# Performance work log

Measured on AMD Instinct MI355X. Metric: run time of the kernel, lower is better.

Reference implementation:

```python
import jax, jax.numpy as jnp
import numpy as np
import math

B, T, F, H = 8, 1024, 1024, 16
D = F // H

def setup_inputs() -> dict:
    key = jax.random.key(0)
    ks = jax.random.split(key, 6)
    s = 1.0 / math.sqrt(F)
    return {
        "qkv": jax.random.normal(ks[0], (B, T, F), dtype=jnp.float32),
        "key_padding_mask": jax.random.randint(ks[1], (B, T), 0, 2).astype(bool),
        "in_proj_w": jax.random.normal(ks[2], (3 * F, F), dtype=jnp.float32) * s,
        "in_proj_b": jax.random.normal(ks[3], (3 * F,), dtype=jnp.float32) * 0.02,
        "out_proj_w": jax.random.normal(ks[4], (F, F), dtype=jnp.float32) * s,
        "out_proj_b": jax.random.normal(ks[5], (F,), dtype=jnp.float32) * 0.02,
    }

def reference(qkv, key_padding_mask, in_proj_w, in_proj_b, out_proj_w, out_proj_b):
    b, t, f = qkv.shape
    h, d = H, f // H
    norm = jnp.asarray(math.sqrt(d), dtype=qkv.dtype)
    # fused QKV projection (torch Linear: x @ W.T + b)
    x = qkv @ in_proj_w.T + in_proj_b                     # [B, T, 3F]
    q, k, v = jnp.split(x, 3, axis=-1)
    q = q.reshape(b, t, h, d).transpose(0, 2, 1, 3)       # [B, H, T, D]
    k = k.reshape(b, t, h, d).transpose(0, 2, 1, 3)
    v = v.reshape(b, t, h, d).transpose(0, 2, 1, 3)
    dot = jnp.einsum("bhqd,bhkd->bhqk", q, k) / norm      # [B, H, T, T]
    dot = jnp.where(key_padding_mask[:, None, None, :], -jnp.inf, dot)
    alpha = jax.nn.softmax(dot, axis=-1)                  # [B, H, T, T]
    att = jnp.einsum("bhqk,bhkd->bhqd", alpha, v)         # [B, H, T, D]
    att = att.transpose(0, 2, 1, 3).reshape(b, t, f)      # [B, T, F]
    out = att @ out_proj_w.T + out_proj_b
    return (out, alpha)
```

## Files before the change

kernel.cpp:

```cpp
#include <hip/hip_runtime.h>
#include <math.h>

#define B_ 8
#define T_ 1024
#define F_ 1024
#define H_ 16
#define D_ 64

typedef __bf16 bf16x8 __attribute__((ext_vector_type(8)));
typedef float f32x4 __attribute__((ext_vector_type(4)));
typedef unsigned short u16x8 __attribute__((ext_vector_type(8)));

__device__ __forceinline__ unsigned short f2bf(float f) {
    union { float f; unsigned u; } v; v.f = f;
    unsigned r = v.u + 0x7fffu + ((v.u >> 16) & 1u);
    return (unsigned short)(r >> 16);
}

__device__ __forceinline__ void gld16(const void* g, void* l) {
    __builtin_amdgcn_global_load_lds(
        (const __attribute__((address_space(1))) void*)g,
        (__attribute__((address_space(3))) void*)l, 16, 0, 0);
}

__device__ __forceinline__ int swz4(int row15) {
    return (row15 ^ (row15 >> 2)) & 3;
}

__global__ __launch_bounds__(256) void cvt_f32_bf16(
    const float* __restrict__ in, unsigned short* __restrict__ out, int n8)
{
    int i = blockIdx.x * 256 + threadIdx.x;
    if (i >= n8) return;
    const float4* p = (const float4*)in + (size_t)i * 2;
    float4 x = p[0], y = p[1];
    u16x8 o;
    o[0] = f2bf(x.x); o[1] = f2bf(x.y); o[2] = f2bf(x.z); o[3] = f2bf(x.w);
    o[4] = f2bf(y.x); o[5] = f2bf(y.y); o[6] = f2bf(y.z); o[7] = f2bf(y.w);
    ((u16x8*)out)[i] = o;
}

__global__ __launch_bounds__(256) void qkv_gemm(
    const unsigned short* __restrict__ A,
    const unsigned short* __restrict__ Bw,
    const float* __restrict__ bias,
    unsigned short* __restrict__ qb,
    unsigned short* __restrict__ kb,
    unsigned short* __restrict__ vb)
{
    __shared__ __align__(16) unsigned short As[128 * 32];
    __shared__ __align__(16) unsigned short Bs[128 * 32];
    const int K = 1024;
    int tid = threadIdx.x;
    int lane = tid & 63, wave = tid >> 6;
    int wr = wave >> 1, wc = wave & 1;
    int m0 = blockIdx.y * 128, n0 = blockIdx.x * 128;
    int col = lane & 15, quad = lane >> 4;
    int sw = swz4(col);
    int rl = lane >> 2;
    int lc = (lane & 3) ^ swz4(rl);

    f32x4 acc[4][4] = {};
    for (int kc = 0; kc < K; kc += 32) {
        __syncthreads();
        #pragma unroll
        for (int l = 0; l < 2; l++) {
            int ia = wave * 2 + l;
            gld16(A  + (size_t)(m0 + ia * 16 + rl) * K + kc + lc * 8, &As[ia * 512]);
            gld16(Bw + (size_t)(n0 + ia * 16 + rl) * K + kc + lc * 8, &Bs[ia * 512]);
        }
        __syncthreads();
        bf16x8 af[4], bg[4];
        #pragma unroll
        for (int mt = 0; mt < 4; mt++)
            af[mt] = *(const bf16x8*)&As[(wr * 64 + mt * 16 + col) * 32 + ((quad ^ sw)) * 8];
        #pragma unroll
        for (int nt = 0; nt < 4; nt++)
            bg[nt] = *(const bf16x8*)&Bs[(wc * 64 + nt * 16 + col) * 32 + ((quad ^ sw)) * 8];
        #pragma unroll
        for (int mt = 0; mt < 4; mt++)
            #pragma unroll
            for (int nt = 0; nt < 4; nt++)
                acc[mt][nt] = __builtin_amdgcn_mfma_f32_16x16x32_bf16(
                    af[mt], bg[nt], acc[mt][nt], 0, 0, 0);
    }
    int which = n0 >> 10;
    #pragma unroll
    for (int nt = 0; nt < 4; nt++) {
        int n = n0 + wc * 64 + nt * 16 + col;
        int hn = (n & 1023) >> 6, d = n & 63;
        float bn = bias[n];
        #pragma unroll
        for (int mt = 0; mt < 4; mt++) {
            #pragma unroll
            for (int r = 0; r < 4; r++) {
                int m = m0 + wr * 64 + mt * 16 + quad * 4 + r;
                int bb = m >> 10, t = m & 1023;
                unsigned short bf = f2bf(acc[mt][nt][r] + bn);
                if (which == 0)
                    qb[(size_t)((bb * H_ + hn) * T_ + t) * D_ + d] = bf;
                else if (which == 1)
                    kb[(size_t)((bb * H_ + hn) * T_ + t) * D_ + d] = bf;
                else
                    vb[(size_t)((bb * H_ + hn) * D_ + d) * T_ + t] = bf;
            }
        }
    }
}

__global__ __launch_bounds__(256) void fused_attn(
    const unsigned short* __restrict__ qb,
    const unsigned short* __restrict__ kb,
    const unsigned short* __restrict__ vb,
    const int* __restrict__ mask,
    float* __restrict__ alpha,
    unsigned short* __restrict__ attb)
{
    __shared__ __align__(16) unsigned short U[16 * 1032];
    __shared__ __align__(16) unsigned short Vs[4][2][1024];
    __shared__ float redmax[4][16];
    __shared__ float redsum[4][16];
    int b = blockIdx.z, h = blockIdx.y, q0 = blockIdx.x * 16;
    int tid = threadIdx.x, lane = tid & 63, wave = tid >> 6;
    int col = lane & 15, quad = lane >> 4;
    const unsigned short* qbase = qb + ((size_t)(b * H_ + h) * T_ + q0) * D_;
    const unsigned short* kbase = kb + ((size_t)(b * H_ + h) * T_) * D_;

    bf16x8 aq0 = *(const bf16x8*)&qbase[col * 64 + quad * 8];
    bf16x8 aq1 = *(const bf16x8*)&qbase[col * 64 + 32 + quad * 8];

    int krl = lane >> 3;
    int klc = (lane & 7) ^ krl;
    int sw8 = col & 7;
    unsigned short* Kb0 = &U[wave * 4096];
    unsigned short* Kb1 = Kb0 + 2048;

    #pragma unroll
    for (int j = 0; j < 4; j++)
        gld16(kbase + (size_t)(wave * 256 + j * 8 + krl) * 64 + klc * 8, Kb0 + j * 512);
    #pragma unroll
    for (int j = 0; j < 4; j++)
        gld16(kbase + (size_t)(wave * 256 + 32 + j * 8 + krl) * 64 + klc * 8, Kb1 + j * 512);

    f32x4 acc[8][2] = {};
    #pragma unroll
    for (int it = 0; it < 8; it++) {
        if (it < 7) { asm volatile("s_waitcnt vmcnt(4)" ::: "memory"); }
        else        { asm volatile("s_waitcnt vmcnt(0)" ::: "memory"); }
        __builtin_amdgcn_sched_barrier(0);
        const unsigned short* Kb = (it & 1) ? Kb1 : Kb0;
        #pragma unroll
        for (int ct = 0; ct < 2; ct++) {
            const unsigned short* kp = Kb + (ct * 16 + col) * 64;
            bf16x8 b0 = *(const bf16x8*)&kp[(quad ^ sw8) * 8];
            bf16x8 b1 = *(const bf16x8*)&kp[((4 + quad) ^ sw8) * 8];
            acc[it][ct] = __builtin_amdgcn_mfma_f32_16x16x32_bf16(aq0, b0, acc[it][ct], 0, 0, 0);
            acc[it][ct] = __builtin_amdgcn_mfma_f32_16x16x32_bf16(aq1, b1, acc[it][ct], 0, 0, 0);
        }
        __builtin_amdgcn_sched_barrier(0);
        if (it < 6) {
            unsigned short* Kn = (it & 1) ? Kb1 : Kb0;
            #pragma unroll
            for (int j = 0; j < 4; j++)
                gld16(kbase + (size_t)(wave * 256 + (it + 2) * 32 + j * 8 + krl) * 64 + klc * 8,
                      Kn + j * 512);
        }
    }

    const unsigned short* vhead = vb + (size_t)(b * H_ + h) * D_ * T_;
    int vrl = lane >> 3;
    int vswz = (lane & 7) ^ vrl;
    #pragma unroll
    for (int i = 0; i < 2; i++)
        gld16(vhead + (size_t)(wave * 16 + i * 8 + vrl) * T_ + vswz * 8, &Vs[wave][0][i * 512]);
    #pragma unroll
    for (int i = 0; i < 2; i++)
        gld16(vhead + (size_t)(wave * 16 + i * 8 + vrl) * T_ + 64 + vswz * 8, &Vs[wave][1][i * 512]);

    const int* mrow = mask + b * T_;
    float mx[4] = {-INFINITY, -INFINITY, -INFINITY, -INFINITY};
    #pragma unroll
    for (int it = 0; it < 8; it++)
        #pragma unroll
        for (int ct = 0; ct < 2; ct++) {
            int k = wave * 256 + it * 32 + ct * 16 + col;
            bool m = mrow[k] != 0;
            #pragma unroll
            for (int r = 0; r < 4; r++) {
                float v = m ? -INFINITY : acc[it][ct][r] * 0.125f;
                acc[it][ct][r] = v;
                mx[r] = fmaxf(mx[r], v);
            }
        }
    #pragma unroll
    for (int r = 0; r < 4; r++) {
        mx[r] = fmaxf(mx[r], __shfl_xor(mx[r], 1, 64));
        mx[r] = fmaxf(mx[r], __shfl_xor(mx[r], 2, 64));
        mx[r] = fmaxf(mx[r], __shfl_xor(mx[r], 4, 64));
        mx[r] = fmaxf(mx[r], __shfl_xor(mx[r], 8, 64));
    }
    if (col == 0)
        #pragma unroll
        for (int r = 0; r < 4; r++) redmax[wave][quad * 4 + r] = mx[r];
    __syncthreads();
    float gm[4];
    #pragma unroll
    for (int r = 0; r < 4; r++) {
        int row = quad * 4 + r;
        gm[r] = fmaxf(fmaxf(redmax[0][row], redmax[1][row]),
                      fmaxf(redmax[2][row], redmax[3][row]));
    }
    float sm[4] = {0.f, 0.f, 0.f, 0.f};
    #pragma unroll
    for (int it = 0; it < 8; it++)
        #pragma unroll
        for (int ct = 0; ct < 2; ct++)
            #pragma unroll
            for (int r = 0; r < 4; r++) {
                float e = __expf(acc[it][ct][r] - gm[r]);
                acc[it][ct][r] = e;
                sm[r] += e;
            }
    #pragma unroll
    for (int r = 0; r < 4; r++) {
        sm[r] += __shfl_xor(sm[r], 1, 64);
        sm[r] += __shfl_xor(sm[r], 2, 64);
        sm[r] += __shfl_xor(sm[r], 4, 64);
        sm[r] += __shfl_xor(sm[r], 8, 64);
    }
    if (col == 0)
        #pragma unroll
        for (int r = 0; r < 4; r++) redsum[wave][quad * 4 + r] = sm[r];
    __syncthreads();
    float inv[4];
    #pragma unroll
    for (int r = 0; r < 4; r++) {
        int row = quad * 4 + r;
        inv[r] = 1.0f / (redsum[0][row] + redsum[1][row] + redsum[2][row] + redsum[3][row]);
    }
    float* abase = alpha + ((size_t)(b * H_ + h) * T_ + q0) * T_;
    #pragma unroll
    for (int it = 0; it < 8; it++)
        #pragma unroll
        for (int ct = 0; ct < 2; ct++) {
            int k = wave * 256 + it * 32 + ct * 16 + col;
            #pragma unroll
            for (int r = 0; r < 4; r++) {
                float v = acc[it][ct][r] * inv[r];
                abase[(size_t)(quad * 4 + r) * T_ + k] = v;
                U[(quad * 4 + r) * 1032 + k] = f2bf(v);
            }
        }
    __syncthreads();
    f32x4 oacc = {};
    #pragma unroll
    for (int t = 0; t < 16; t++) {
        if (t < 15) { asm volatile("s_waitcnt vmcnt(2)" ::: "memory"); }
        else        { asm volatile("s_waitcnt vmcnt(0)" ::: "memory"); }
        __builtin_amdgcn_sched_barrier(0);
        const unsigned short* Vb = Vs[wave][t & 1];
        bf16x8 pa0 = *(const bf16x8*)&U[col * 1032 + t * 64 + quad * 8];
        bf16x8 pa1 = *(const bf16x8*)&U[col * 1032 + t * 64 + 32 + quad * 8];
        bf16x8 bv0 = *(const bf16x8*)&Vb[col * 64 + ((quad ^ sw8)) * 8];
        bf16x8 bv1 = *(const bf16x8*)&Vb[col * 64 + (((quad + 4) ^ sw8)) * 8];
        oacc = __builtin_amdgcn_mfma_f32_16x16x32_bf16(pa0, bv0, oacc, 0, 0, 0);
        oacc = __builtin_amdgcn_mfma_f32_16x16x32_bf16(pa1, bv1, oacc, 0, 0, 0);
        __builtin_amdgcn_sched_barrier(0);
        if (t < 14) {
            #pragma unroll
            for (int i = 0; i < 2; i++)
                gld16(vhead + (size_t)(wave * 16 + i * 8 + vrl) * T_ + (t + 2) * 64 + vswz * 8,
                      &Vs[wave][t & 1][i * 512]);
        }
    }
    #pragma unroll
    for (int r = 0; r < 4; r++) {
        int t = q0 + quad * 4 + r;
        attb[(size_t)(b * T_ + t) * F_ + h * D_ + wave * 16 + col] = f2bf(oacc[r]);
    }
}

__global__ __launch_bounds__(256) void out_gemm(
    const unsigned short* __restrict__ A,
    const unsigned short* __restrict__ Bw,
    const float* __restrict__ bias,
    float* __restrict__ out)
{
    __shared__ __align__(16) unsigned short As[128 * 32];
    __shared__ __align__(16) unsigned short Bs[128 * 32];
    const int K = 1024;
    int tid = threadIdx.x;
    int lane = tid & 63, wave = tid >> 6;
    int wr = wave >> 1, wc = wave & 1;
    int m0 = blockIdx.y * 128, n0 = blockIdx.x * 128;
    int col = lane & 15, quad = lane >> 4;
    int sw = swz4(col);
    int rl = lane >> 2;
    int lc = (lane & 3) ^ swz4(rl);
    f32x4 acc[4][4] = {};
    for (int kc = 0; kc < K; kc += 32) {
        __syncthreads();
        #pragma unroll
        for (int l = 0; l < 2; l++) {
            int ia = wave * 2 + l;
            gld16(A  + (size_t)(m0 + ia * 16 + rl) * K + kc + lc * 8, &As[ia * 512]);
            gld16(Bw + (size_t)(n0 + ia * 16 + rl) * K + kc + lc * 8, &Bs[ia * 512]);
        }
        __syncthreads();
        bf16x8 af[4], bg[4];
        #pragma unroll
        for (int mt = 0; mt < 4; mt++)
            af[mt] = *(const bf16x8*)&As[(wr * 64 + mt * 16 + col) * 32 + ((quad ^ sw)) * 8];
        #pragma unroll
        for (int nt = 0; nt < 4; nt++)
            bg[nt] = *(const bf16x8*)&Bs[(wc * 64 + nt * 16 + col) * 32 + ((quad ^ sw)) * 8];
        #pragma unroll
        for (int mt = 0; mt < 4; mt++)
            #pragma unroll
            for (int nt = 0; nt < 4; nt++)
                acc[mt][nt] = __builtin_amdgcn_mfma_f32_16x16x32_bf16(
                    af[mt], bg[nt], acc[mt][nt], 0, 0, 0);
    }
    #pragma unroll
    for (int nt = 0; nt < 4; nt++) {
        int n = n0 + wc * 64 + nt * 16 + col;
        float bn = bias[n];
        #pragma unroll
        for (int mt = 0; mt < 4; mt++) {
            #pragma unroll
            for (int r = 0; r < 4; r++) {
                int m = m0 + wr * 64 + mt * 16 + quad * 4 + r;
                out[(size_t)m * F_ + n] = acc[mt][nt][r] + bn;
            }
        }
    }
}

extern "C" void kernel_launch(void* const* d_in, const int* in_sizes, int n_in,
                              void* d_out, int out_size, void* d_ws, size_t ws_size,
                              hipStream_t stream)
{
    const float* qkv   = (const float*)d_in[0];
    const int*   mask  = (const int*)d_in[1];
    const float* in_w  = (const float*)d_in[2];
    const float* in_b  = (const float*)d_in[3];
    const float* out_w = (const float*)d_in[4];
    const float* out_b = (const float*)d_in[5];
    float* out = (float*)d_out;
    const size_t NE = (size_t)B_ * T_ * F_;
    float* alpha = out + NE;

    unsigned short* ws   = (unsigned short*)d_ws;
    unsigned short* Xb   = ws;
    unsigned short* Wib  = Xb  + NE;
    unsigned short* Wob  = Wib + 3 * F_ * F_;
    unsigned short* qb2  = Wob + (size_t)F_ * F_;
    unsigned short* kb2  = qb2 + NE;
    unsigned short* vb2  = kb2 + NE;
    unsigned short* attb = vb2 + NE;

    cvt_f32_bf16<<<dim3((int)(NE / 8 / 256)), 256, 0, stream>>>(qkv, Xb, (int)(NE / 8));
    cvt_f32_bf16<<<dim3(3 * F_ * F_ / 8 / 256), 256, 0, stream>>>(in_w, Wib, 3 * F_ * F_ / 8);
    cvt_f32_bf16<<<dim3(F_ * F_ / 8 / 256), 256, 0, stream>>>(out_w, Wob, F_ * F_ / 8);

    qkv_gemm<<<dim3(24, 64), 256, 0, stream>>>(Xb, Wib, in_b, qb2, kb2, vb2);
    fused_attn<<<dim3(64, H_, B_), 256, 0, stream>>>(qb2, kb2, vb2, mask, alpha, attb);
    out_gemm<<<dim3(8, 64), 256, 0, stream>>>(attb, Wob, out_b, out);
}
```

Baseline: 905.8 us.

## Triple-buffer GEMM LDS loads, remap tile order, and merge conversion kernels

Both projection GEMMs now use a three-stage LDS ring filled by async global-to-LDS loads issued two k-steps ahead. Each step waits with vmcnt and a single barrier instead of two syncthreads, so load latency can overlap the MFMA work. Tile indices are remapped so that blocks launched together share nearby rows and columns, which should improve L2 reuse. The three fp32-to-bf16 conversion launches are merged into one kernel. The cost is three times the LDS per block, which may lower occupancy, and waitcnt logic that depends on the exact number of outstanding loads.

```diff
diff --git a/kernel.cpp b/kernel.cpp
--- a/kernel.cpp
+++ b/kernel.cpp
@@ -27,11 +27,16 @@
     return (row15 ^ (row15 >> 2)) & 3;
 }
 
-__global__ __launch_bounds__(256) void cvt_f32_bf16(
-    const float* __restrict__ in, unsigned short* __restrict__ out, int n8)
+__global__ __launch_bounds__(256) void cvt3(
+    const float* __restrict__ a, unsigned short* __restrict__ oa, int na8,
+    const float* __restrict__ b, unsigned short* __restrict__ ob, int nb8,
+    const float* __restrict__ c, unsigned short* __restrict__ oc, int nc8)
 {
     int i = blockIdx.x * 256 + threadIdx.x;
-    if (i >= n8) return;
+    const float* in; unsigned short* out;
+    if (i < na8)            { in = a; out = oa; }
+    else if (i < na8 + nb8) { in = b; out = ob; i -= na8; }
+    else                    { in = c; out = oc; i -= na8 + nb8; if (i >= nc8) return; }
     const float4* p = (const float4*)in + (size_t)i * 2;
     float4 x = p[0], y = p[1];
     u16x8 o;
@@ -48,42 +53,77 @@
     unsigned short* __restrict__ kb,
     unsigned short* __restrict__ vb)
 {
-    __shared__ __align__(16) unsigned short As[128 * 32];
-    __shared__ __align__(16) unsigned short Bs[128 * 32];
+    __shared__ __align__(16) unsigned short As[3][128 * 32];
+    __shared__ __align__(16) unsigned short Bs[3][128 * 32];
     const int K = 1024;
     int tid = threadIdx.x;
     int lane = tid & 63, wave = tid >> 6;
     int wr = wave >> 1, wc = wave & 1;
-    int m0 = blockIdx.y * 128, n0 = blockIdx.x * 128;
+    int l = blockIdx.y * 24 + blockIdx.x;
+    int s = (l & 7) * 192 + (l >> 3);
+    int m0 = (s / 24) * 128, n0 = (s % 24) * 128;
     int col = lane & 15, quad = lane >> 4;
     int sw = swz4(col);
     int rl = lane >> 2;
     int lc = (lane & 3) ^ swz4(rl);
 
+    #define QKV_STAGE(ri, kt) do {                                              \
+        int kc_ = (kt) * 32;                                                    \
+        _Pragma("unroll")                                                       \
+        for (int ld = 0; ld < 2; ld++) {                                        \
+            int ia = wave * 2 + ld;                                             \
+            gld16(A  + (size_t)(m0 + ia * 16 + rl) * K + kc_ + lc * 8,          \
+                  &As[ri][ia * 512]);                                           \
+            gld16(Bw + (size_t)(n0 + ia * 16 + rl) * K + kc_ + lc * 8,          \
+                  &Bs[ri][ia * 512]);                                           \
+        }                                                                       \
+    } while (0)
+
+    QKV_STAGE(0, 0);
+    QKV_STAGE(1, 1);
+
     f32x4 acc[4][4] = {};
-    for (int kc = 0; kc < K; kc += 32) {
-        __syncthreads();
-        #pragma unroll
-        for (int l = 0; l < 2; l++) {
-            int ia = wave * 2 + l;
-            gld16(A  + (size_t)(m0 + ia * 16 + rl) * K + kc + lc * 8, &As[ia * 512]);
-            gld16(Bw + (size_t)(n0 + ia * 16 + rl) * K + kc + lc * 8, &Bs[ia * 512]);
-        }
-        __syncthreads();
+    int ri = 0;
+    for (int t = 0; t < 31; t++) {
+        asm volatile("s_waitcnt vmcnt(4)" ::: "memory");
+        __builtin_amdgcn_sched_barrier(0);
+        __builtin_amdgcn_s_barrier();
         bf16x8 af[4], bg[4];
         #pragma unroll
         for (int mt = 0; mt < 4; mt++)
-            af[mt] = *(const bf16x8*)&As[(wr * 64 + mt * 16 + col) * 32 + ((quad ^ sw)) * 8];
+            af[mt] = *(const bf16x8*)&As[ri][(wr * 64 + mt * 16 + col) * 32 + (quad ^ sw) * 8];
         #pragma unroll
         for (int nt = 0; nt < 4; nt++)
-            bg[nt] = *(const bf16x8*)&Bs[(wc * 64 + nt * 16 + col) * 32 + ((quad ^ sw)) * 8];
+            bg[nt] = *(const bf16x8*)&Bs[ri][(wc * 64 + nt * 16 + col) * 32 + (quad ^ sw) * 8];
+        int rn = ri + 2; if (rn >= 3) rn -= 3;
+        if (t < 30) QKV_STAGE(rn, t + 2);
         #pragma unroll
         for (int mt = 0; mt < 4; mt++)
             #pragma unroll
             for (int nt = 0; nt < 4; nt++)
                 acc[mt][nt] = __builtin_amdgcn_mfma_f32_16x16x32_bf16(
                     af[mt], bg[nt], acc[mt][nt], 0, 0, 0);
-    }
+        ri = ri + 1; if (ri >= 3) ri -= 3;
+    }
+    {
+        asm volatile("s_waitcnt vmcnt(0)" ::: "memory");
+        __builtin_amdgcn_sched_barrier(0);
+        __builtin_amdgcn_s_barrier();
+        bf16x8 af[4], bg[4];
+        #pragma unroll
+        for (int mt = 0; mt < 4; mt++)
+            af[mt] = *(const bf16x8*)&As[ri][(wr * 64 + mt * 16 + col) * 32 + (quad ^ sw) * 8];
+        #pragma unroll
+        for (int nt = 0; nt < 4; nt++)
+            bg[nt] = *(const bf16x8*)&Bs[ri][(wc * 64 + nt * 16 + col) * 32 + (quad ^ sw) * 8];
+        #pragma unroll
+        for (int mt = 0; mt < 4; mt++)
+            #pragma unroll
+            for (int nt = 0; nt < 4; nt++)
+                acc[mt][nt] = __builtin_amdgcn_mfma_f32_16x16x32_bf16(
+                    af[mt], bg[nt], acc[mt][nt], 0, 0, 0);
+    }
+    #undef QKV_STAGE
     int which = n0 >> 10;
     #pragma unroll
     for (int nt = 0; nt < 4; nt++) {
@@ -286,41 +326,77 @@
     const float* __restrict__ bias,
     float* __restrict__ out)
 {
-    __shared__ __align__(16) unsigned short As[128 * 32];
-    __shared__ __align__(16) unsigned short Bs[128 * 32];
+    __shared__ __align__(16) unsigned short As[3][128 * 32];
+    __shared__ __align__(16) unsigned short Bs[3][128 * 32];
     const int K = 1024;
     int tid = threadIdx.x;
     int lane = tid & 63, wave = tid >> 6;
     int wr = wave >> 1, wc = wave & 1;
-    int m0 = blockIdx.y * 128, n0 = blockIdx.x * 128;
+    int l = blockIdx.y * 8 + blockIdx.x;
+    int s = (l & 7) * 64 + (l >> 3);
+    int m0 = (s / 8) * 128, n0 = (s % 8) * 128;
     int col = lane & 15, quad = lane >> 4;
     int sw = swz4(col);
     int rl = lane >> 2;
     int lc = (lane & 3) ^ swz4(rl);
+
+    #define OUT_STAGE(ri, kt) do {                                              \
+        int kc_ = (kt) * 32;                                                    \
+        _Pragma("unroll")                                                       \
+        for (int ld = 0; ld < 2; ld++) {                                        \
+            int ia = wave * 2 + ld;                                             \
+            gld16(A  + (size_t)(m0 + ia * 16 + rl) * K + kc_ + lc * 8,          \
+                  &As[ri][ia * 512]);                                           \
+            gld16(Bw + (size_t)(n0 + ia * 16 + rl) * K + kc_ + lc * 8,          \
+                  &Bs[ri][ia * 512]);                                           \
+        }                                                                       \
+    } while (0)
+
+    OUT_STAGE(0, 0);
+    OUT_STAGE(1, 1);
+
     f32x4 acc[4][4] = {};
-    for (int kc = 0; kc < K; kc += 32) {
-        __syncthreads();
-        #pragma unroll
-        for (int l = 0; l < 2; l++) {
-            int ia = wave * 2 + l;
-            gld16(A  + (size_t)(m0 + ia * 16 + rl) * K + kc + lc * 8, &As[ia * 512]);
-            gld16(Bw + (size_t)(n0 + ia * 16 + rl) * K + kc + lc * 8, &Bs[ia * 512]);
-        }
-        __syncthreads();
+    int ri = 0;
+    for (int t = 0; t < 31; t++) {
+        asm volatile("s_waitcnt vmcnt(4)" ::: "memory");
+        __builtin_amdgcn_sched_barrier(0);
+        __builtin_amdgcn_s_barrier();
         bf16x8 af[4], bg[4];
         #pragma unroll
         for (int mt = 0; mt < 4; mt++)
-            af[mt] = *(const bf16x8*)&As[(wr * 64 + mt * 16 + col) * 32 + ((quad ^ sw)) * 8];
+            af[mt] = *(const bf16x8*)&As[ri][(wr * 64 + mt * 16 + col) * 32 + (quad ^ sw) * 8];
         #pragma unroll
         for (int nt = 0; nt < 4; nt++)
-            bg[nt] = *(const bf16x8*)&Bs[(wc * 64 + nt * 16 + col) * 32 + ((quad ^ sw)) * 8];
+            bg[nt] = *(const bf16x8*)&Bs[ri][(wc * 64 + nt * 16 + col) * 32 + (quad ^ sw) * 8];
+        int rn = ri + 2; if (rn >= 3) rn -= 3;
+        if (t < 30) OUT_STAGE(rn, t + 2);
         #pragma unroll
         for (int mt = 0; mt < 4; mt++)
             #pragma unroll
             for (int nt = 0; nt < 4; nt++)
                 acc[mt][nt] = __builtin_amdgcn_mfma_f32_16x16x32_bf16(
                     af[mt], bg[nt], acc[mt][nt], 0, 0, 0);
-    }
+        ri = ri + 1; if (ri >= 3) ri -= 3;
+    }
+    {
+        asm volatile("s_waitcnt vmcnt(0)" ::: "memory");
+        __builtin_amdgcn_sched_barrier(0);
+        __builtin_amdgcn_s_barrier();
+        bf16x8 af[4], bg[4];
+        #pragma unroll
+        for (int mt = 0; mt < 4; mt++)
+            af[mt] = *(const bf16x8*)&As[ri][(wr * 64 + mt * 16 + col) * 32 + (quad ^ sw) * 8];
+        #pragma unroll
+        for (int nt = 0; nt < 4; nt++)
+            bg[nt] = *(const bf16x8*)&Bs[ri][(wc * 64 + nt * 16 + col) * 32 + (quad ^ sw) * 8];
+        #pragma unroll
+        for (int mt = 0; mt < 4; mt++)
+            #pragma unroll
+            for (int nt = 0; nt < 4; nt++)
+                acc[mt][nt] = __builtin_amdgcn_mfma_f32_16x16x32_bf16(
+                    af[mt], bg[nt], acc[mt][nt], 0, 0, 0);
+    }
+    #undef OUT_STAGE
     #pragma unroll
     for (int nt = 0; nt < 4; nt++) {
         int n = n0 + wc * 64 + nt * 16 + col;
@@ -359,9 +435,11 @@
     unsigned short* vb2  = kb2 + NE;
     unsigned short* attb = vb2 + NE;
 
-    cvt_f32_bf16<<<dim3((int)(NE / 8 / 256)), 256, 0, stream>>>(qkv, Xb, (int)(NE / 8));
-    cvt_f32_bf16<<<dim3(3 * F_ * F_ / 8 / 256), 256, 0, stream>>>(in_w, Wib, 3 * F_ * F_ / 8);
-    cvt_f32_bf16<<<dim3(F_ * F_ / 8 / 256), 256, 0, stream>>>(out_w, Wob, F_ * F_ / 8);
+    const int na8 = (int)(NE / 8);
+    const int nb8 = 3 * F_ * F_ / 8;
+    const int nc8 = F_ * F_ / 8;
+    cvt3<<<dim3((na8 + nb8 + nc8) / 256), 256, 0, stream>>>(
+        qkv, Xb, na8, in_w, Wib, nb8, out_w, Wob, nc8);
 
     qkv_gemm<<<dim3(24, 64), 256, 0, stream>>>(Xb, Wib, in_b, qb2, kb2, vb2);
     fused_attn<<<dim3(64, H_, B_), 256, 0, stream>>>(qb2, kb2, vb2, mask, alpha, attb);
```

Result: no change. 902.7 us (-0.3%).
